# Kernel tuning notes

Hardware: AMD Instinct MI355X
Metric: run time of the kernel (lower is better)

The kernel has to match this reference:

```python
import jax, jax.numpy as jnp
import numpy as np

N_NODES = 100000
N_EDGES = 1600000
N_LAYERS = 3
DIM = 128


def setup_inputs() -> dict:
    key = jax.random.key(0)
    k1, k2, k3, k4 = jax.random.split(key, 4)
    x = jax.random.normal(k1, (N_NODES, DIM), dtype=jnp.float32)
    edge_indices = jax.random.randint(k2, (N_LAYERS, 2, N_EDGES), 0, N_NODES, dtype=jnp.int64)
    # GCNConv weight (glorot-ish scale) and bias per layer; all layers are DIM->DIM
    W = jax.random.normal(k3, (N_LAYERS, DIM, DIM), dtype=jnp.float32) * (1.0 / np.sqrt(DIM))
    b = jax.random.normal(k4, (N_LAYERS, DIM), dtype=jnp.float32) * 0.01
    return {"x": x, "edge_indices": edge_indices, "W": W, "b": b}


def _gcn_layer(x, edge_index, W_l, b_l):
    # Module does vstack((ei[1], ei[0])) then flow='target_to_source', which is
    # equivalent to standard GCNConv (source_to_target) on the original edge_index.
    N = x.shape[0]
    loop = jnp.arange(N, dtype=edge_index.dtype)  # self loops (add_self_loops=True)
    row = jnp.concatenate([edge_index[0], loop])  # message sources
    col = jnp.concatenate([edge_index[1], loop])  # aggregation targets
    ones = jnp.ones(row.shape[0], dtype=x.dtype)
    deg = jax.ops.segment_sum(ones, col, num_segments=N)  # in-degree incl. self loop
    dis = jax.lax.rsqrt(jnp.maximum(deg, 1.0))  # deg >= 1 due to self loops
    norm = dis[row] * dis[col]  # [E+N]
    h = x @ W_l  # linear (no bias inside GCNConv's lin)
    agg = jax.ops.segment_sum(h[row] * norm[:, None], col, num_segments=N)
    return agg + b_l


def reference(x, edge_indices, W, b):
    # eval mode: dropout(p=0.5) between layers is identity
    for l in range(edge_indices.shape[0]):
        x = jax.nn.relu(_gcn_layer(x, edge_indices[l], W[l], b[l]))
    return x
```

## Files before the change

kernel.cpp:

```cpp
#include <hip/hip_runtime.h>

#define DIM 128
#define NB_MAX 512
#define CAP_B 4608
#define TILE_EDGES 4096
#define PT 512
#define EPT (TILE_EDGES / PT)

typedef int idx_t;

typedef __bf16 bf16x8 __attribute__((ext_vector_type(8)));
typedef float f32x4 __attribute__((ext_vector_type(4)));

static __device__ __forceinline__ unsigned int f2bf(float f) {
    unsigned int u = __float_as_uint(f);
    return (u + 0x7fffu + ((u >> 16) & 1u)) >> 16;
}
static __device__ __forceinline__ float bf2f(unsigned int hi) {
    return __uint_as_float(hi << 16);
}

__global__ void k_zero_i(int* __restrict__ p, int n) {
    int i = blockIdx.x * blockDim.x + threadIdx.x;
    if (i < n) p[i] = 0;
}

__global__ __launch_bounds__(PT) void k_partition3(const idx_t* __restrict__ edges,
                                                   int* __restrict__ gcur_all,
                                                   unsigned int* __restrict__ pairs_all,
                                                   int E, int NB) {
    const int l = blockIdx.y;
    const idx_t* row = edges + (size_t)l * 2 * E;
    const idx_t* col = row + E;
    int* gcur = gcur_all + l * NB_MAX;
    unsigned int* pairs = pairs_all + (size_t)l * NB * CAP_B;

    __shared__ int s_cnt[NB_MAX];
    __shared__ int s_base[NB_MAX];
    __shared__ int s_res[NB_MAX];
    __shared__ int s_scan[PT];
    __shared__ unsigned int s_stage[TILE_EDGES];
    __shared__ unsigned int s_gdst[TILE_EDGES];

    const int tid = threadIdx.x;
    const int base_e = blockIdx.x * TILE_EDGES;
    const int cnt_total = min(TILE_EDGES, E - base_e);

    for (int b = tid; b < NB; b += PT) s_cnt[b] = 0;
    __syncthreads();

    int myb[EPT];
    unsigned int mypk[EPT];
    #pragma unroll
    for (int i = 0; i < EPT; ++i) {
        int e = base_e + tid + i * PT;
        if (e < E) {
            int c = col[e];
            myb[i] = c >> 8;
            mypk[i] = ((unsigned int)row[e] << 8) | (unsigned int)(c & 255);
            atomicAdd(&s_cnt[myb[i]], 1);
        } else {
            myb[i] = -1;
        }
    }
    __syncthreads();

    int v = (tid < NB) ? s_cnt[tid] : 0;
    s_scan[tid] = v;
    __syncthreads();
    for (int off = 1; off < PT; off <<= 1) {
        int t = (tid >= off) ? s_scan[tid - off] : 0;
        __syncthreads();
        s_scan[tid] += t;
        __syncthreads();
    }
    if (tid < NB) {
        s_base[tid] = s_scan[tid] - v;
        s_res[tid] = v ? atomicAdd(&gcur[tid], v) : 0;
        s_cnt[tid] = 0;
    }
    __syncthreads();

    #pragma unroll
    for (int i = 0; i < EPT; ++i) {
        if (myb[i] >= 0) {
            int b = myb[i];
            int li = atomicAdd(&s_cnt[b], 1);
            int slot = s_base[b] + li;
            int g = s_res[b] + li;
            s_stage[slot] = mypk[i];
            s_gdst[slot] = (g < CAP_B) ? (unsigned int)(b * CAP_B + g) : 0xFFFFFFFFu;
        }
    }
    __syncthreads();

    for (int s = tid; s < cnt_total; s += PT) {
        unsigned int d = s_gdst[s];
        if (d != 0xFFFFFFFFu) pairs[d] = s_stage[s];
    }
}

__global__ __launch_bounds__(256) void k_local_sort3(const unsigned int* __restrict__ pairs_all,
                                                     const int* __restrict__ gcur_all,
                                                     int* __restrict__ srow_all,
                                                     int* __restrict__ offs_all,
                                                     int* __restrict__ ends_all,
                                                     float* __restrict__ dis_all,
                                                     int NB, int N) {
    const int l = blockIdx.y;
    const unsigned int* pairs = pairs_all + (size_t)l * NB * CAP_B;
    const int* gcur = gcur_all + l * NB_MAX;
    int* srow = srow_all + (size_t)l * NB * CAP_B;
    int* offs = offs_all + (size_t)l * N;
    int* ends = ends_all + (size_t)l * N;
    float* dis = dis_all + (size_t)l * N;

    __shared__ int hist[256];
    __shared__ int loffs_s[256];
    __shared__ int lcur[256];
    __shared__ int rows_s[CAP_B];
    const int tid = threadIdx.x;
    const int b = blockIdx.x;
    const int lo = b * CAP_B;
    int n = gcur[b];
    if (n > CAP_B) n = CAP_B;
    const int node0 = b << 8;

    hist[tid] = 0;
    __syncthreads();
    for (int i = tid; i < n; i += 256)
        atomicAdd(&hist[pairs[lo + i] & 255u], 1);
    __syncthreads();

    int v = hist[tid];
    loffs_s[tid] = v;
    __syncthreads();
    for (int off = 1; off < 256; off <<= 1) {
        int t = (tid >= off) ? loffs_s[tid - off] : 0;
        __syncthreads();
        loffs_s[tid] += t;
        __syncthreads();
    }
    int excl = loffs_s[tid] - v;
    loffs_s[tid] = excl;
    lcur[tid] = 0;
    int node = node0 + tid;
    if (node < N) {
        offs[node] = lo + excl;
        ends[node] = lo + excl + v;
        dis[node] = rsqrtf((float)(v + 1));
    }
    __syncthreads();

    for (int i = tid; i < n; i += 256) {
        unsigned int pk = pairs[lo + i];
        int c = pk & 255u;
        int p = loffs_s[c] + atomicAdd(&lcur[c], 1);
        rows_s[p] = (int)(pk >> 8);
    }
    __syncthreads();
    for (int i = tid; i < n; i += 256) srow[lo + i] = rows_s[i];
}

template <bool BF16IN>
__global__ __launch_bounds__(512) void k_gemm_mfma(const void* __restrict__ xin,
                                                   const float* __restrict__ W,
                                                   unsigned int* __restrict__ hb,
                                                   int M) {
    __shared__ alignas(16) unsigned short Ah[128 * 32];
    __shared__ alignas(16) unsigned short Al[128 * 32];

    const int tid  = threadIdx.x;
    const int lane = tid & 63;
    const int wv   = tid >> 6;
    const int col0 = wv * 16;
    const int row0 = blockIdx.x * 128;

    union U8 { unsigned short u[8]; bf16x8 v; };
    bf16x8 Bh[4], Bl[4];
    {
        const int bcol = col0 + (lane & 15);
        #pragma unroll
        for (int t = 0; t < 4; ++t) {
            U8 uh, ul;
            #pragma unroll
            for (int j = 0; j < 8; ++j) {
                int k = t * 32 + (lane >> 4) * 8 + j;
                float w = W[k * DIM + bcol];
                unsigned int hi = f2bf(w);
                uh.u[j] = (unsigned short)hi;
                ul.u[j] = (unsigned short)f2bf(w - bf2f(hi));
            }
            Bh[t] = uh.v;
            Bl[t] = ul.v;
        }
    }

    f32x4 acc[8];
    #pragma unroll
    for (int m = 0; m < 8; ++m) acc[m] = (f32x4){0.f, 0.f, 0.f, 0.f};

    const int srow_ = tid >> 2;
    const int quad  = tid & 3;
    const int gr    = row0 + srow_;
    const int sidx  = (srow_ * 32 + quad * 8) ^ ((srow_ & 7) << 3);

    for (int t = 0; t < 4; ++t) {
        if constexpr (BF16IN) {
            const unsigned int* xb = (const unsigned int*)xin;
            uint4 v = make_uint4(0, 0, 0, 0);
            if (gr < M) v = *(const uint4*)&xb[(size_t)gr * 64 + t * 16 + quad * 4];
            __syncthreads();
            *(uint4*)&Ah[sidx] = v;
            __syncthreads();
        } else {
            const float* x = (const float*)xin;
            float f[8];
            if (gr < M) {
                const float4* xp = (const float4*)&x[(size_t)gr * DIM + t * 32 + quad * 8];
                float4 v0 = xp[0], v1 = xp[1];
                f[0] = v0.x; f[1] = v0.y; f[2] = v0.z; f[3] = v0.w;
                f[4] = v1.x; f[5] = v1.y; f[6] = v1.z; f[7] = v1.w;
            } else {
                #pragma unroll
                for (int j = 0; j < 8; ++j) f[j] = 0.0f;
            }
            unsigned int ph[4], pl[4];
            #pragma unroll
            for (int j = 0; j < 4; ++j) {
                unsigned int h0 = f2bf(f[2 * j]),     l0 = f2bf(f[2 * j] - bf2f(h0));
                unsigned int h1 = f2bf(f[2 * j + 1]), l1 = f2bf(f[2 * j + 1] - bf2f(h1));
                ph[j] = h0 | (h1 << 16);
                pl[j] = l0 | (l1 << 16);
            }
            __syncthreads();
            *(uint4*)&Ah[sidx] = make_uint4(ph[0], ph[1], ph[2], ph[3]);
            *(uint4*)&Al[sidx] = make_uint4(pl[0], pl[1], pl[2], pl[3]);
            __syncthreads();
        }

        #pragma unroll
        for (int m = 0; m < 8; ++m) {
            int lrow = m * 16 + (lane & 15);
            int idx = (lrow * 32 + (lane >> 4) * 8) ^ ((lrow & 7) << 3);
            bf16x8 ah = *(const bf16x8*)&Ah[idx];
            acc[m] = __builtin_amdgcn_mfma_f32_16x16x32_bf16(ah, Bh[t], acc[m], 0, 0, 0);
            acc[m] = __builtin_amdgcn_mfma_f32_16x16x32_bf16(ah, Bl[t], acc[m], 0, 0, 0);
            if constexpr (!BF16IN) {
                bf16x8 al = *(const bf16x8*)&Al[idx];
                acc[m] = __builtin_amdgcn_mfma_f32_16x16x32_bf16(al, Bh[t], acc[m], 0, 0, 0);
            }
        }
    }

    const int lane15 = lane & 15;
    #pragma unroll
    for (int m = 0; m < 8; ++m) {
        #pragma unroll
        for (int r = 0; r < 4; ++r) {
            float v = acc[m][r];
            float vp = __shfl_xor(v, 1);
            int grow = row0 + m * 16 + (lane >> 4) * 4 + r;
            if (!(lane15 & 1) && grow < M) {
                unsigned int p = f2bf(v) | (f2bf(vp) << 16);
                hb[(size_t)grow * 64 + wv * 8 + (lane15 >> 1)] = p;
            }
        }
    }
}

template <bool OUT_BF16>
__global__ __launch_bounds__(256) void k_aggregate(const unsigned int* __restrict__ hb,
                                                   const float* __restrict__ dis,
                                                   const int* __restrict__ offs,
                                                   const int* __restrict__ ends,
                                                   const int* __restrict__ srow,
                                                   const float* __restrict__ b,
                                                   void* __restrict__ outv, int N) {
    int node = blockIdx.x * 4 + (threadIdx.x >> 6);
    if (node >= N) return;
    int lane = threadIdx.x & 63;

    float dn = dis[node];
    unsigned int hv = hb[(size_t)node * 64 + lane];
    float ax0 = __uint_as_float(hv << 16) * dn * dn;
    float ay0 = __uint_as_float(hv & 0xffff0000u) * dn * dn;
    float ax1 = 0.f, ay1 = 0.f, ax2 = 0.f, ay2 = 0.f, ax3 = 0.f, ay3 = 0.f;

    int j = offs[node];
    const int end = ends[node];

    for (; j + 8 <= end; j += 8) {
        int r0 = srow[j],     r1 = srow[j + 1], r2 = srow[j + 2], r3 = srow[j + 3];
        int r4 = srow[j + 4], r5 = srow[j + 5], r6 = srow[j + 6], r7 = srow[j + 7];
        float w0 = dis[r0] * dn, w1 = dis[r1] * dn, w2 = dis[r2] * dn, w3 = dis[r3] * dn;
        float w4 = dis[r4] * dn, w5 = dis[r5] * dn, w6 = dis[r6] * dn, w7 = dis[r7] * dn;
        unsigned int a0 = hb[(size_t)r0 * 64 + lane];
        unsigned int a1 = hb[(size_t)r1 * 64 + lane];
        unsigned int a2 = hb[(size_t)r2 * 64 + lane];
        unsigned int a3 = hb[(size_t)r3 * 64 + lane];
        unsigned int a4 = hb[(size_t)r4 * 64 + lane];
        unsigned int a5 = hb[(size_t)r5 * 64 + lane];
        unsigned int a6 = hb[(size_t)r6 * 64 + lane];
        unsigned int a7 = hb[(size_t)r7 * 64 + lane];
        ax0 += __uint_as_float(a0 << 16) * w0; ay0 += __uint_as_float(a0 & 0xffff0000u) * w0;
        ax1 += __uint_as_float(a1 << 16) * w1; ay1 += __uint_as_float(a1 & 0xffff0000u) * w1;
        ax2 += __uint_as_float(a2 << 16) * w2; ay2 += __uint_as_float(a2 & 0xffff0000u) * w2;
        ax3 += __uint_as_float(a3 << 16) * w3; ay3 += __uint_as_float(a3 & 0xffff0000u) * w3;
        ax0 += __uint_as_float(a4 << 16) * w4; ay0 += __uint_as_float(a4 & 0xffff0000u) * w4;
        ax1 += __uint_as_float(a5 << 16) * w5; ay1 += __uint_as_float(a5 & 0xffff0000u) * w5;
        ax2 += __uint_as_float(a6 << 16) * w6; ay2 += __uint_as_float(a6 & 0xffff0000u) * w6;
        ax3 += __uint_as_float(a7 << 16) * w7; ay3 += __uint_as_float(a7 & 0xffff0000u) * w7;
    }
    for (; j + 2 <= end; j += 2) {
        int r0 = srow[j], r1 = srow[j + 1];
        float w0 = dis[r0] * dn, w1 = dis[r1] * dn;
        unsigned int a0 = hb[(size_t)r0 * 64 + lane];
        unsigned int a1 = hb[(size_t)r1 * 64 + lane];
        ax0 += __uint_as_float(a0 << 16) * w0; ay0 += __uint_as_float(a0 & 0xffff0000u) * w0;
        ax1 += __uint_as_float(a1 << 16) * w1; ay1 += __uint_as_float(a1 & 0xffff0000u) * w1;
    }
    if (j < end) {
        int r = srow[j];
        float w = dis[r] * dn;
        unsigned int a = hb[(size_t)r * 64 + lane];
        ax0 += __uint_as_float(a << 16) * w; ay0 += __uint_as_float(a & 0xffff0000u) * w;
    }

    float2 bb = ((const float2*)b)[lane];
    float ox = (ax0 + ax1) + (ax2 + ax3) + bb.x;
    float oy = (ay0 + ay1) + (ay2 + ay3) + bb.y;
    ox = ox > 0.0f ? ox : 0.0f;
    oy = oy > 0.0f ? oy : 0.0f;
    if constexpr (OUT_BF16) {
        ((unsigned int*)outv)[(size_t)node * 64 + lane] = f2bf(ox) | (f2bf(oy) << 16);
    } else {
        ((float2*)outv)[(size_t)node * 64 + lane] = make_float2(ox, oy);
    }
}

extern "C" void kernel_launch(void* const* d_in, const int* in_sizes, int n_in,
                              void* d_out, int out_size, void* d_ws, size_t ws_size,
                              hipStream_t stream) {
    const float* x     = (const float*)d_in[0];
    const idx_t* edges = (const idx_t*)d_in[1];
    const float* W     = (const float*)d_in[2];
    const float* b     = (const float*)d_in[3];

    const int N = in_sizes[0] / DIM;
    const int E = in_sizes[1] / 6;
    const int NB = (N + 255) >> 8;
    const size_t PADE = (size_t)NB * CAP_B;

    char* ws = (char*)d_ws;
    auto align = [](size_t v) { return (v + 255) & ~(size_t)255; };
    size_t o = 0;
    float* dis3   = (float*)(ws + o); o = align(o + (size_t)3 * N * 4);
    int*   offs3  = (int*)(ws + o);   o = align(o + (size_t)3 * N * 4);
    int*   ends3  = (int*)(ws + o);   o = align(o + (size_t)3 * N * 4);
    int*   gcur3  = (int*)(ws + o);   o = align(o + (size_t)3 * NB_MAX * 4);
    int*   srow3  = (int*)(ws + o);   o = align(o + (size_t)3 * PADE * 4);
    unsigned int* hb   = (unsigned int*)(ws + o); o = align(o + (size_t)N * 64 * 4);
    unsigned int* bufA = (unsigned int*)(ws + o); o = align(o + (size_t)N * 64 * 4);
    unsigned int* pairs3 = hb;

    const int T = 256;
    const int gAg = (N + 3) / 4;
    const int gGemm = (N + 127) / 128;
    const int gPart = (E + TILE_EDGES - 1) / TILE_EDGES;

    k_zero_i<<<(3 * NB_MAX + T - 1) / T, T, 0, stream>>>(gcur3, 3 * NB_MAX);
    k_partition3<<<dim3(gPart, 3), PT, 0, stream>>>(edges, gcur3, pairs3, E, NB);
    k_local_sort3<<<dim3(NB, 3), T, 0, stream>>>(pairs3, gcur3, srow3, offs3, ends3,
                                                 dis3, NB, N);

    k_gemm_mfma<false><<<gGemm, 512, 0, stream>>>(x, W, hb, N);
    k_aggregate<true><<<gAg, T, 0, stream>>>(hb, dis3, offs3, ends3, srow3, b, bufA, N);

    k_gemm_mfma<true><<<gGemm, 512, 0, stream>>>(bufA, W + (size_t)DIM * DIM, hb, N);
    k_aggregate<true><<<gAg, T, 0, stream>>>(hb, dis3 + N, offs3 + N, ends3 + N,
                                             srow3 + PADE, b + DIM, bufA, N);

    k_gemm_mfma<true><<<gGemm, 512, 0, stream>>>(bufA, W + (size_t)2 * DIM * DIM, hb, N);
    k_aggregate<false><<<gAg, T, 0, stream>>>(hb, dis3 + 2 * (size_t)N,
                                              offs3 + 2 * (size_t)N, ends3 + 2 * (size_t)N,
                                              srow3 + 2 * PADE, b + 2 * DIM,
                                              d_out, N);
}
```

Measured before the change: 318.8 us.

## Slice GEMM output into 8 column slabs and aggregate per slab

The GEMM now writes its bf16 output as 8 separate column slabs of 16 features each (32 bytes per node), not one 256-byte row per node. The aggregation kernel assigns 8 lanes per node within one slab, and consecutive blocks of 8 cover the slabs for the same 32 nodes. The aim is a smaller gather working set per pass so the slab fits better in L2/MALL and improves cache hit rates on random neighbour rows. The trade-off is that the edge list, dis lookups and index loads are now read 8 times instead of once, and each gather is only 32 bytes wide.

```diff
diff --git a/kernel.cpp b/kernel.cpp
--- a/kernel.cpp
+++ b/kernel.cpp
@@ -254,6 +254,7 @@
     }
 
     const int lane15 = lane & 15;
+    const size_t sl_base = (size_t)wv * M * 8;
     #pragma unroll
     for (int m = 0; m < 8; ++m) {
         #pragma unroll
@@ -263,26 +264,30 @@
             int grow = row0 + m * 16 + (lane >> 4) * 4 + r;
             if (!(lane15 & 1) && grow < M) {
                 unsigned int p = f2bf(v) | (f2bf(vp) << 16);
-                hb[(size_t)grow * 64 + wv * 8 + (lane15 >> 1)] = p;
+                hb[sl_base + (size_t)grow * 8 + (lane15 >> 1)] = p;
             }
         }
     }
 }
 
 template <bool OUT_BF16>
-__global__ __launch_bounds__(256) void k_aggregate(const unsigned int* __restrict__ hb,
-                                                   const float* __restrict__ dis,
-                                                   const int* __restrict__ offs,
-                                                   const int* __restrict__ ends,
-                                                   const int* __restrict__ srow,
-                                                   const float* __restrict__ b,
-                                                   void* __restrict__ outv, int N) {
-    int node = blockIdx.x * 4 + (threadIdx.x >> 6);
+__global__ __launch_bounds__(256) void k_aggregate_s(const unsigned int* __restrict__ hb,
+                                                     const float* __restrict__ dis,
+                                                     const int* __restrict__ offs,
+                                                     const int* __restrict__ ends,
+                                                     const int* __restrict__ srow,
+                                                     const float* __restrict__ bia,
+                                                     void* __restrict__ outv, int N) {
+    const int s   = blockIdx.x & 7;
+    const int nb  = blockIdx.x >> 3;
+    const int tid = threadIdx.x;
+    const int li  = tid & 7;
+    const int node = nb * 32 + (tid >> 3);
     if (node >= N) return;
-    int lane = threadIdx.x & 63;
+    const unsigned int* hs = hb + (size_t)s * N * 8;
 
     float dn = dis[node];
-    unsigned int hv = hb[(size_t)node * 64 + lane];
+    unsigned int hv = hs[(size_t)node * 8 + li];
     float ax0 = __uint_as_float(hv << 16) * dn * dn;
     float ay0 = __uint_as_float(hv & 0xffff0000u) * dn * dn;
     float ax1 = 0.f, ay1 = 0.f, ax2 = 0.f, ay2 = 0.f, ax3 = 0.f, ay3 = 0.f;
@@ -290,52 +295,44 @@
     int j = offs[node];
     const int end = ends[node];
 
-    for (; j + 8 <= end; j += 8) {
-        int r0 = srow[j],     r1 = srow[j + 1], r2 = srow[j + 2], r3 = srow[j + 3];
-        int r4 = srow[j + 4], r5 = srow[j + 5], r6 = srow[j + 6], r7 = srow[j + 7];
-        float w0 = dis[r0] * dn, w1 = dis[r1] * dn, w2 = dis[r2] * dn, w3 = dis[r3] * dn;
-        float w4 = dis[r4] * dn, w5 = dis[r5] * dn, w6 = dis[r6] * dn, w7 = dis[r7] * dn;
-        unsigned int a0 = hb[(size_t)r0 * 64 + lane];
-        unsigned int a1 = hb[(size_t)r1 * 64 + lane];
-        unsigned int a2 = hb[(size_t)r2 * 64 + lane];
-        unsigned int a3 = hb[(size_t)r3 * 64 + lane];
-        unsigned int a4 = hb[(size_t)r4 * 64 + lane];
-        unsigned int a5 = hb[(size_t)r5 * 64 + lane];
-        unsigned int a6 = hb[(size_t)r6 * 64 + lane];
-        unsigned int a7 = hb[(size_t)r7 * 64 + lane];
+    for (; j + 4 <= end; j += 4) {
+        int r0 = srow[j], r1 = srow[j + 1], r2 = srow[j + 2], r3 = srow[j + 3];
+        float w0 = dis[r0] * dn, w1 = dis[r1] * dn;
+        float w2 = dis[r2] * dn, w3 = dis[r3] * dn;
+        unsigned int a0 = hs[(size_t)r0 * 8 + li];
+        unsigned int a1 = hs[(size_t)r1 * 8 + li];
+        unsigned int a2 = hs[(size_t)r2 * 8 + li];
+        unsigned int a3 = hs[(size_t)r3 * 8 + li];
         ax0 += __uint_as_float(a0 << 16) * w0; ay0 += __uint_as_float(a0 & 0xffff0000u) * w0;
         ax1 += __uint_as_float(a1 << 16) * w1; ay1 += __uint_as_float(a1 & 0xffff0000u) * w1;
         ax2 += __uint_as_float(a2 << 16) * w2; ay2 += __uint_as_float(a2 & 0xffff0000u) * w2;
         ax3 += __uint_as_float(a3 << 16) * w3; ay3 += __uint_as_float(a3 & 0xffff0000u) * w3;
-        ax0 += __uint_as_float(a4 << 16) * w4; ay0 += __uint_as_float(a4 & 0xffff0000u) * w4;
-        ax1 += __uint_as_float(a5 << 16) * w5; ay1 += __uint_as_float(a5 & 0xffff0000u) * w5;
-        ax2 += __uint_as_float(a6 << 16) * w6; ay2 += __uint_as_float(a6 & 0xffff0000u) * w6;
-        ax3 += __uint_as_float(a7 << 16) * w7; ay3 += __uint_as_float(a7 & 0xffff0000u) * w7;
-    }
-    for (; j + 2 <= end; j += 2) {
+    }
+    if (j + 2 <= end) {
         int r0 = srow[j], r1 = srow[j + 1];
         float w0 = dis[r0] * dn, w1 = dis[r1] * dn;
-        unsigned int a0 = hb[(size_t)r0 * 64 + lane];
-        unsigned int a1 = hb[(size_t)r1 * 64 + lane];
+        unsigned int a0 = hs[(size_t)r0 * 8 + li];
+        unsigned int a1 = hs[(size_t)r1 * 8 + li];
         ax0 += __uint_as_float(a0 << 16) * w0; ay0 += __uint_as_float(a0 & 0xffff0000u) * w0;
         ax1 += __uint_as_float(a1 << 16) * w1; ay1 += __uint_as_float(a1 & 0xffff0000u) * w1;
+        j += 2;
     }
     if (j < end) {
         int r = srow[j];
         float w = dis[r] * dn;
-        unsigned int a = hb[(size_t)r * 64 + lane];
-        ax0 += __uint_as_float(a << 16) * w; ay0 += __uint_as_float(a & 0xffff0000u) * w;
-    }
-
-    float2 bb = ((const float2*)b)[lane];
+        unsigned int a = hs[(size_t)r * 8 + li];
+        ax2 += __uint_as_float(a << 16) * w; ay2 += __uint_as_float(a & 0xffff0000u) * w;
+    }
+
+    float2 bb = ((const float2*)bia)[s * 8 + li];
     float ox = (ax0 + ax1) + (ax2 + ax3) + bb.x;
     float oy = (ay0 + ay1) + (ay2 + ay3) + bb.y;
     ox = ox > 0.0f ? ox : 0.0f;
     oy = oy > 0.0f ? oy : 0.0f;
     if constexpr (OUT_BF16) {
-        ((unsigned int*)outv)[(size_t)node * 64 + lane] = f2bf(ox) | (f2bf(oy) << 16);
+        ((unsigned int*)outv)[(size_t)node * 64 + s * 8 + li] = f2bf(ox) | (f2bf(oy) << 16);
     } else {
-        ((float2*)outv)[(size_t)node * 64 + lane] = make_float2(ox, oy);
+        ((float2*)outv)[(size_t)node * 64 + s * 8 + li] = make_float2(ox, oy);
     }
 }
 
@@ -365,7 +362,7 @@
     unsigned int* pairs3 = hb;
 
     const int T = 256;
-    const int gAg = (N + 3) / 4;
+    const int gAgS = ((N + 31) / 32) * 8;
     const int gGemm = (N + 127) / 128;
     const int gPart = (E + TILE_EDGES - 1) / TILE_EDGES;
 
@@ -375,15 +372,15 @@
                                                  dis3, NB, N);
 
     k_gemm_mfma<false><<<gGemm, 512, 0, stream>>>(x, W, hb, N);
-    k_aggregate<true><<<gAg, T, 0, stream>>>(hb, dis3, offs3, ends3, srow3, b, bufA, N);
+    k_aggregate_s<true><<<gAgS, T, 0, stream>>>(hb, dis3, offs3, ends3, srow3, b, bufA, N);
 
     k_gemm_mfma<true><<<gGemm, 512, 0, stream>>>(bufA, W + (size_t)DIM * DIM, hb, N);
-    k_aggregate<true><<<gAg, T, 0, stream>>>(hb, dis3 + N, offs3 + N, ends3 + N,
-                                             srow3 + PADE, b + DIM, bufA, N);
+    k_aggregate_s<true><<<gAgS, T, 0, stream>>>(hb, dis3 + N, offs3 + N, ends3 + N,
+                                                srow3 + PADE, b + DIM, bufA, N);
 
     k_gemm_mfma<true><<<gGemm, 512, 0, stream>>>(bufA, W + (size_t)2 * DIM * DIM, hb, N);
-    k_aggregate<false><<<gAg, T, 0, stream>>>(hb, dis3 + 2 * (size_t)N,
-                                              offs3 + 2 * (size_t)N, ends3 + 2 * (size_t)N,
-                                              srow3 + 2 * PADE, b + 2 * DIM,
-                                              d_out, N);
-}
+    k_aggregate_s<false><<<gAgS, T, 0, stream>>>(hb, dis3 + 2 * (size_t)N,
+                                                 offs3 + 2 * (size_t)N, ends3 + 2 * (size_t)N,
+                                                 srow3 + 2 * PADE, b + 2 * DIM,
+                                                 d_out, N);
+}
```

Measured after the change: 522.9 us. 64.0% more time.

## Fuse edge partition with first-layer GEMM into one heterogeneous launch

Applied to the files above, without the earlier changes.

Merges the edge-partition kernel and the first fp32-input GEMM into a single launch: a block index decides whether a block partitions edges or computes a GEMM tile, and a shared-memory union holds both layouts. The pairs scratch moves from hb to bufA so the two jobs can run at once, removing one launch and letting the memory-bound partition overlap with MFMA work. The local sort now uses 512 threads and stages pairs in LDS so global memory is read only once. The larger union LDS footprint may lower occupancy for the GEMM blocks.

```diff
diff --git a/kernel.cpp b/kernel.cpp
--- a/kernel.cpp
+++ b/kernel.cpp
@@ -5,6 +5,7 @@
 #define CAP_B 4608
 #define TILE_EDGES 4096
 #define PT 512
+#define ST 512
 #define EPT (TILE_EDGES / PT)
 
 typedef int idx_t;
@@ -25,28 +26,37 @@
     if (i < n) p[i] = 0;
 }
 
-__global__ __launch_bounds__(PT) void k_partition3(const idx_t* __restrict__ edges,
-                                                   int* __restrict__ gcur_all,
-                                                   unsigned int* __restrict__ pairs_all,
-                                                   int E, int NB) {
-    const int l = blockIdx.y;
+struct PartSM {
+    int s_cnt[NB_MAX];
+    int s_base[NB_MAX];
+    int s_res[NB_MAX];
+    int s_scan[PT];
+    unsigned int s_stage[TILE_EDGES];
+    unsigned int s_gdst[TILE_EDGES];
+};
+struct GemmSM {
+    alignas(16) unsigned short Ah[128 * 32];
+    alignas(16) unsigned short Al[128 * 32];
+};
+union SMem { PartSM p; GemmSM g; };
+
+static __device__ void partition_body(PartSM& sm,
+                                      const idx_t* __restrict__ edges,
+                                      int* __restrict__ gcur_all,
+                                      unsigned int* __restrict__ pairs_all,
+                                      int E, int NB, int pb, int gPart) {
+    const int l  = pb / gPart;
+    const int bx = pb % gPart;
     const idx_t* row = edges + (size_t)l * 2 * E;
     const idx_t* col = row + E;
     int* gcur = gcur_all + l * NB_MAX;
     unsigned int* pairs = pairs_all + (size_t)l * NB * CAP_B;
 
-    __shared__ int s_cnt[NB_MAX];
-    __shared__ int s_base[NB_MAX];
-    __shared__ int s_res[NB_MAX];
-    __shared__ int s_scan[PT];
-    __shared__ unsigned int s_stage[TILE_EDGES];
-    __shared__ unsigned int s_gdst[TILE_EDGES];
-
     const int tid = threadIdx.x;
-    const int base_e = blockIdx.x * TILE_EDGES;
+    const int base_e = bx * TILE_EDGES;
     const int cnt_total = min(TILE_EDGES, E - base_e);
 
-    for (int b = tid; b < NB; b += PT) s_cnt[b] = 0;
+    for (int b = tid; b < NB; b += PT) sm.s_cnt[b] = 0;
     __syncthreads();
 
     int myb[EPT];
@@ -58,26 +68,26 @@
             int c = col[e];
             myb[i] = c >> 8;
             mypk[i] = ((unsigned int)row[e] << 8) | (unsigned int)(c & 255);
-            atomicAdd(&s_cnt[myb[i]], 1);
+            atomicAdd(&sm.s_cnt[myb[i]], 1);
         } else {
             myb[i] = -1;
         }
     }
     __syncthreads();
 
-    int v = (tid < NB) ? s_cnt[tid] : 0;
-    s_scan[tid] = v;
+    int v = (tid < NB) ? sm.s_cnt[tid] : 0;
+    sm.s_scan[tid] = v;
     __syncthreads();
     for (int off = 1; off < PT; off <<= 1) {
-        int t = (tid >= off) ? s_scan[tid - off] : 0;
-        __syncthreads();
-        s_scan[tid] += t;
+        int t = (tid >= off) ? sm.s_scan[tid - off] : 0;
+        __syncthreads();
+        sm.s_scan[tid] += t;
         __syncthreads();
     }
     if (tid < NB) {
-        s_base[tid] = s_scan[tid] - v;
-        s_res[tid] = v ? atomicAdd(&gcur[tid], v) : 0;
-        s_cnt[tid] = 0;
+        sm.s_base[tid] = sm.s_scan[tid] - v;
+        sm.s_res[tid] = v ? atomicAdd(&gcur[tid], v) : 0;
+        sm.s_cnt[tid] = 0;
     }
     __syncthreads();
 
@@ -85,96 +95,31 @@
     for (int i = 0; i < EPT; ++i) {
         if (myb[i] >= 0) {
             int b = myb[i];
-            int li = atomicAdd(&s_cnt[b], 1);
-            int slot = s_base[b] + li;
-            int g = s_res[b] + li;
-            s_stage[slot] = mypk[i];
-            s_gdst[slot] = (g < CAP_B) ? (unsigned int)(b * CAP_B + g) : 0xFFFFFFFFu;
+            int li = atomicAdd(&sm.s_cnt[b], 1);
+            int slot = sm.s_base[b] + li;
+            int g = sm.s_res[b] + li;
+            sm.s_stage[slot] = mypk[i];
+            sm.s_gdst[slot] = (g < CAP_B) ? (unsigned int)(b * CAP_B + g) : 0xFFFFFFFFu;
         }
     }
     __syncthreads();
 
     for (int s = tid; s < cnt_total; s += PT) {
-        unsigned int d = s_gdst[s];
-        if (d != 0xFFFFFFFFu) pairs[d] = s_stage[s];
-    }
-}
-
-__global__ __launch_bounds__(256) void k_local_sort3(const unsigned int* __restrict__ pairs_all,
-                                                     const int* __restrict__ gcur_all,
-                                                     int* __restrict__ srow_all,
-                                                     int* __restrict__ offs_all,
-                                                     int* __restrict__ ends_all,
-                                                     float* __restrict__ dis_all,
-                                                     int NB, int N) {
-    const int l = blockIdx.y;
-    const unsigned int* pairs = pairs_all + (size_t)l * NB * CAP_B;
-    const int* gcur = gcur_all + l * NB_MAX;
-    int* srow = srow_all + (size_t)l * NB * CAP_B;
-    int* offs = offs_all + (size_t)l * N;
-    int* ends = ends_all + (size_t)l * N;
-    float* dis = dis_all + (size_t)l * N;
-
-    __shared__ int hist[256];
-    __shared__ int loffs_s[256];
-    __shared__ int lcur[256];
-    __shared__ int rows_s[CAP_B];
-    const int tid = threadIdx.x;
-    const int b = blockIdx.x;
-    const int lo = b * CAP_B;
-    int n = gcur[b];
-    if (n > CAP_B) n = CAP_B;
-    const int node0 = b << 8;
-
-    hist[tid] = 0;
-    __syncthreads();
-    for (int i = tid; i < n; i += 256)
-        atomicAdd(&hist[pairs[lo + i] & 255u], 1);
-    __syncthreads();
-
-    int v = hist[tid];
-    loffs_s[tid] = v;
-    __syncthreads();
-    for (int off = 1; off < 256; off <<= 1) {
-        int t = (tid >= off) ? loffs_s[tid - off] : 0;
-        __syncthreads();
-        loffs_s[tid] += t;
-        __syncthreads();
-    }
-    int excl = loffs_s[tid] - v;
-    loffs_s[tid] = excl;
-    lcur[tid] = 0;
-    int node = node0 + tid;
-    if (node < N) {
-        offs[node] = lo + excl;
-        ends[node] = lo + excl + v;
-        dis[node] = rsqrtf((float)(v + 1));
-    }
-    __syncthreads();
-
-    for (int i = tid; i < n; i += 256) {
-        unsigned int pk = pairs[lo + i];
-        int c = pk & 255u;
-        int p = loffs_s[c] + atomicAdd(&lcur[c], 1);
-        rows_s[p] = (int)(pk >> 8);
-    }
-    __syncthreads();
-    for (int i = tid; i < n; i += 256) srow[lo + i] = rows_s[i];
-}
-
-template <bool BF16IN>
-__global__ __launch_bounds__(512) void k_gemm_mfma(const void* __restrict__ xin,
-                                                   const float* __restrict__ W,
-                                                   unsigned int* __restrict__ hb,
-                                                   int M) {
-    __shared__ alignas(16) unsigned short Ah[128 * 32];
-    __shared__ alignas(16) unsigned short Al[128 * 32];
-
+        unsigned int d = sm.s_gdst[s];
+        if (d != 0xFFFFFFFFu) pairs[d] = sm.s_stage[s];
+    }
+}
+
+static __device__ void gemm0_body(GemmSM& sm,
+                                  const float* __restrict__ x,
+                                  const float* __restrict__ W,
+                                  unsigned int* __restrict__ hb,
+                                  int M, int bx) {
     const int tid  = threadIdx.x;
     const int lane = tid & 63;
     const int wv   = tid >> 6;
     const int col0 = wv * 16;
-    const int row0 = blockIdx.x * 128;
+    const int row0 = bx * 128;
 
     union U8 { unsigned short u[8]; bf16x8 v; };
     bf16x8 Bh[4], Bl[4];
@@ -206,38 +151,187 @@
     const int sidx  = (srow_ * 32 + quad * 8) ^ ((srow_ & 7) << 3);
 
     for (int t = 0; t < 4; ++t) {
-        if constexpr (BF16IN) {
-            const unsigned int* xb = (const unsigned int*)xin;
-            uint4 v = make_uint4(0, 0, 0, 0);
-            if (gr < M) v = *(const uint4*)&xb[(size_t)gr * 64 + t * 16 + quad * 4];
-            __syncthreads();
-            *(uint4*)&Ah[sidx] = v;
-            __syncthreads();
+        float f[8];
+        if (gr < M) {
+            const float4* xp = (const float4*)&x[(size_t)gr * DIM + t * 32 + quad * 8];
+            float4 v0 = xp[0], v1 = xp[1];
+            f[0] = v0.x; f[1] = v0.y; f[2] = v0.z; f[3] = v0.w;
+            f[4] = v1.x; f[5] = v1.y; f[6] = v1.z; f[7] = v1.w;
         } else {
-            const float* x = (const float*)xin;
-            float f[8];
-            if (gr < M) {
-                const float4* xp = (const float4*)&x[(size_t)gr * DIM + t * 32 + quad * 8];
-                float4 v0 = xp[0], v1 = xp[1];
-                f[0] = v0.x; f[1] = v0.y; f[2] = v0.z; f[3] = v0.w;
-                f[4] = v1.x; f[5] = v1.y; f[6] = v1.z; f[7] = v1.w;
-            } else {
-                #pragma unroll
-                for (int j = 0; j < 8; ++j) f[j] = 0.0f;
+            #pragma unroll
+            for (int j = 0; j < 8; ++j) f[j] = 0.0f;
+        }
+        unsigned int ph[4], pl[4];
+        #pragma unroll
+        for (int j = 0; j < 4; ++j) {
+            unsigned int h0 = f2bf(f[2 * j]),     l0 = f2bf(f[2 * j] - bf2f(h0));
+            unsigned int h1 = f2bf(f[2 * j + 1]), l1 = f2bf(f[2 * j + 1] - bf2f(h1));
+            ph[j] = h0 | (h1 << 16);
+            pl[j] = l0 | (l1 << 16);
+        }
+        __syncthreads();
+        *(uint4*)&sm.Ah[sidx] = make_uint4(ph[0], ph[1], ph[2], ph[3]);
+        *(uint4*)&sm.Al[sidx] = make_uint4(pl[0], pl[1], pl[2], pl[3]);
+        __syncthreads();
+
+        #pragma unroll
+        for (int m = 0; m < 8; ++m) {
+            int lrow = m * 16 + (lane & 15);
+            int idx = (lrow * 32 + (lane >> 4) * 8) ^ ((lrow & 7) << 3);
+            bf16x8 ah = *(const bf16x8*)&sm.Ah[idx];
+            bf16x8 al = *(const bf16x8*)&sm.Al[idx];
+            acc[m] = __builtin_amdgcn_mfma_f32_16x16x32_bf16(ah, Bh[t], acc[m], 0, 0, 0);
+            acc[m] = __builtin_amdgcn_mfma_f32_16x16x32_bf16(ah, Bl[t], acc[m], 0, 0, 0);
+            acc[m] = __builtin_amdgcn_mfma_f32_16x16x32_bf16(al, Bh[t], acc[m], 0, 0, 0);
+        }
+    }
+
+    const int lane15 = lane & 15;
+    #pragma unroll
+    for (int m = 0; m < 8; ++m) {
+        #pragma unroll
+        for (int r = 0; r < 4; ++r) {
+            float v = acc[m][r];
+            float vp = __shfl_xor(v, 1);
+            int grow = row0 + m * 16 + (lane >> 4) * 4 + r;
+            if (!(lane15 & 1) && grow < M) {
+                unsigned int p = f2bf(v) | (f2bf(vp) << 16);
+                hb[(size_t)grow * 64 + wv * 8 + (lane15 >> 1)] = p;
             }
-            unsigned int ph[4], pl[4];
+        }
+    }
+}
+
+__global__ __launch_bounds__(PT) void k_fused0(const float* __restrict__ x,
+                                               const float* __restrict__ W,
+                                               unsigned int* __restrict__ hb, int M,
+                                               const idx_t* __restrict__ edges,
+                                               int* __restrict__ gcur_all,
+                                               unsigned int* __restrict__ pairs_all,
+                                               int E, int NB, int gPart, int partBlocks) {
+    __shared__ SMem sm;
+    const int pb = blockIdx.x;
+    if (pb < partBlocks)
+        partition_body(sm.p, edges, gcur_all, pairs_all, E, NB, pb, gPart);
+    else
+        gemm0_body(sm.g, x, W, hb, M, pb - partBlocks);
+}
+
+__global__ __launch_bounds__(ST) void k_local_sort3(const unsigned int* __restrict__ pairs_all,
+                                                    const int* __restrict__ gcur_all,
+                                                    int* __restrict__ srow_all,
+                                                    int* __restrict__ offs_all,
+                                                    int* __restrict__ ends_all,
+                                                    float* __restrict__ dis_all,
+                                                    int NB, int N) {
+    const int l = blockIdx.y;
+    const unsigned int* pairs = pairs_all + (size_t)l * NB * CAP_B;
+    const int* gcur = gcur_all + l * NB_MAX;
+    int* srow = srow_all + (size_t)l * NB * CAP_B;
+    int* offs = offs_all + (size_t)l * N;
+    int* ends = ends_all + (size_t)l * N;
+    float* dis = dis_all + (size_t)l * N;
+
+    __shared__ int hist[256];
+    __shared__ int loffs_s[256];
+    __shared__ int lcur[256];
+    __shared__ unsigned int stage[CAP_B];
+    __shared__ int rows_s[CAP_B];
+    const int tid = threadIdx.x;
+    const int b = blockIdx.x;
+    const int lo = b * CAP_B;
+    int n = gcur[b];
+    if (n > CAP_B) n = CAP_B;
+    const int node0 = b << 8;
+
+    if (tid < 256) hist[tid] = 0;
+    __syncthreads();
+    for (int i = tid; i < n; i += ST) {
+        unsigned int pk = pairs[lo + i];
+        stage[i] = pk;
+        atomicAdd(&hist[pk & 255u], 1);
+    }
+    __syncthreads();
+
+    int v = (tid < 256) ? hist[tid] : 0;
+    if (tid < 256) loffs_s[tid] = v;
+    __syncthreads();
+    for (int off = 1; off < 256; off <<= 1) {
+        int t = (tid >= off && tid < 256) ? loffs_s[tid - off] : 0;
+        __syncthreads();
+        if (tid < 256) loffs_s[tid] += t;
+        __syncthreads();
+    }
+    if (tid < 256) {
+        int excl = loffs_s[tid] - v;
+        loffs_s[tid] = excl;
+        lcur[tid] = 0;
+        int node = node0 + tid;
+        if (node < N) {
+            offs[node] = lo + excl;
+            ends[node] = lo + excl + v;
+            dis[node] = rsqrtf((float)(v + 1));
+        }
+    }
+    __syncthreads();
+
+    for (int i = tid; i < n; i += ST) {
+        unsigned int pk = stage[i];
+        int c = pk & 255u;
+        int p = loffs_s[c] + atomicAdd(&lcur[c], 1);
+        rows_s[p] = (int)(pk >> 8);
+    }
+    __syncthreads();
+    for (int i = tid; i < n; i += ST) srow[lo + i] = rows_s[i];
+}
+
+__global__ __launch_bounds__(512) void k_gemm_bf16(const unsigned int* __restrict__ xb,
+                                                   const float* __restrict__ W,
+                                                   unsigned int* __restrict__ hb,
+                                                   int M) {
+    __shared__ alignas(16) unsigned short Ah[128 * 32];
+
+    const int tid  = threadIdx.x;
+    const int lane = tid & 63;
+    const int wv   = tid >> 6;
+    const int col0 = wv * 16;
+    const int row0 = blockIdx.x * 128;
+
+    union U8 { unsigned short u[8]; bf16x8 v; };
+    bf16x8 Bh[4], Bl[4];
+    {
+        const int bcol = col0 + (lane & 15);
+        #pragma unroll
+        for (int t = 0; t < 4; ++t) {
+            U8 uh, ul;
             #pragma unroll
-            for (int j = 0; j < 4; ++j) {
-                unsigned int h0 = f2bf(f[2 * j]),     l0 = f2bf(f[2 * j] - bf2f(h0));
-                unsigned int h1 = f2bf(f[2 * j + 1]), l1 = f2bf(f[2 * j + 1] - bf2f(h1));
-                ph[j] = h0 | (h1 << 16);
-                pl[j] = l0 | (l1 << 16);
+            for (int j = 0; j < 8; ++j) {
+                int k = t * 32 + (lane >> 4) * 8 + j;
+                float w = W[k * DIM + bcol];
+                unsigned int hi = f2bf(w);
+                uh.u[j] = (unsigned short)hi;
+                ul.u[j] = (unsigned short)f2bf(w - bf2f(hi));
             }
-            __syncthreads();
-            *(uint4*)&Ah[sidx] = make_uint4(ph[0], ph[1], ph[2], ph[3]);
-            *(uint4*)&Al[sidx] = make_uint4(pl[0], pl[1], pl[2], pl[3]);
-            __syncthreads();
-        }
+            Bh[t] = uh.v;
+            Bl[t] = ul.v;
+        }
+    }
+
+    f32x4 acc[8];
+    #pragma unroll
+    for (int m = 0; m < 8; ++m) acc[m] = (f32x4){0.f, 0.f, 0.f, 0.f};
+
+    const int srow_ = tid >> 2;
+    const int quad  = tid & 3;
+    const int gr    = row0 + srow_;
+    const int sidx  = (srow_ * 32 + quad * 8) ^ ((srow_ & 7) << 3);
+
+    for (int t = 0; t < 4; ++t) {
+        uint4 v = make_uint4(0, 0, 0, 0);
+        if (gr < M) v = *(const uint4*)&xb[(size_t)gr * 64 + t * 16 + quad * 4];
+        __syncthreads();
+        *(uint4*)&Ah[sidx] = v;
+        __syncthreads();
 
         #pragma unroll
         for (int m = 0; m < 8; ++m) {
@@ -246,10 +340,6 @@
             bf16x8 ah = *(const bf16x8*)&Ah[idx];
             acc[m] = __builtin_amdgcn_mfma_f32_16x16x32_bf16(ah, Bh[t], acc[m], 0, 0, 0);
             acc[m] = __builtin_amdgcn_mfma_f32_16x16x32_bf16(ah, Bl[t], acc[m], 0, 0, 0);
-            if constexpr (!BF16IN) {
-                bf16x8 al = *(const bf16x8*)&Al[idx];
-                acc[m] = __builtin_amdgcn_mfma_f32_16x16x32_bf16(al, Bh[t], acc[m], 0, 0, 0);
-            }
         }
     }
 
@@ -362,26 +452,27 @@
     int*   srow3  = (int*)(ws + o);   o = align(o + (size_t)3 * PADE * 4);
     unsigned int* hb   = (unsigned int*)(ws + o); o = align(o + (size_t)N * 64 * 4);
     unsigned int* bufA = (unsigned int*)(ws + o); o = align(o + (size_t)N * 64 * 4);
-    unsigned int* pairs3 = hb;
+    unsigned int* pairs3 = bufA;
 
     const int T = 256;
     const int gAg = (N + 3) / 4;
     const int gGemm = (N + 127) / 128;
     const int gPart = (E + TILE_EDGES - 1) / TILE_EDGES;
+    const int partBlocks = 3 * gPart;
 
     k_zero_i<<<(3 * NB_MAX + T - 1) / T, T, 0, stream>>>(gcur3, 3 * NB_MAX);
-    k_partition3<<<dim3(gPart, 3), PT, 0, stream>>>(edges, gcur3, pairs3, E, NB);
-    k_local_sort3<<<dim3(NB, 3), T, 0, stream>>>(pairs3, gcur3, srow3, offs3, ends3,
-                                                 dis3, NB, N);
-
-    k_gemm_mfma<false><<<gGemm, 512, 0, stream>>>(x, W, hb, N);
+    k_fused0<<<partBlocks + gGemm, PT, 0, stream>>>(x, W, hb, N, edges, gcur3,
+                                                    pairs3, E, NB, gPart, partBlocks);
+    k_local_sort3<<<dim3(NB, 3), ST, 0, stream>>>(pairs3, gcur3, srow3, offs3, ends3,
+                                                  dis3, NB, N);
+
     k_aggregate<true><<<gAg, T, 0, stream>>>(hb, dis3, offs3, ends3, srow3, b, bufA, N);
 
-    k_gemm_mfma<true><<<gGemm, 512, 0, stream>>>(bufA, W + (size_t)DIM * DIM, hb, N);
+    k_gemm_bf16<<<gGemm, 512, 0, stream>>>(bufA, W + (size_t)DIM * DIM, hb, N);
     k_aggregate<true><<<gAg, T, 0, stream>>>(hb, dis3 + N, offs3 + N, ends3 + N,
                                              srow3 + PADE, b + DIM, bufA, N);
 
-    k_gemm_mfma<true><<<gGemm, 512, 0, stream>>>(bufA, W + (size_t)2 * DIM * DIM, hb, N);
+    k_gemm_bf16<<<gGemm, 512, 0, stream>>>(bufA, W + (size_t)2 * DIM * DIM, hb, N);
     k_aggregate<false><<<gAg, T, 0, stream>>>(hb, dis3 + 2 * (size_t)N,
                                               offs3 + 2 * (size_t)N, ends3 + 2 * (size_t)N,
                                               srow3 + 2 * PADE, b + 2 * DIM,
```

Result: no change. 312.8 us (-1.9%).
